# Optimization experiments

Measured on AMD Instinct MI355X. Metric: run time of the kernel, lower is better.

Reference implementation:

```python
import jax, jax.numpy as jnp
import numpy as np

N_ELEC = 8192   # electrons (nodes)
N_NUC = 512     # nuclei
EMB = 256       # embedding_dim
KER = 256       # kernel_dim
DF = 64         # dist_feat_dim
MID = 128       # round(sqrt(DF*KER)), log-interpolated hidden width of w-MLP
E = 131072      # edges per edge type


def _ssp(x):
    # shifted softplus, deepqmc default activation: log(0.5*exp(x) + 0.5)
    return jax.nn.softplus(x) - jnp.log(2.0)


def setup_inputs() -> dict:
    key = jax.random.key(0)
    ks = jax.random.split(key, 24)
    def nrm(k, shape, scale):
        return jax.random.normal(k, shape, dtype=jnp.float32) * scale
    inp = {}
    inp['electrons'] = nrm(ks[0], (N_ELEC, EMB), 1.0)
    inp['nuclei'] = nrm(ks[1], (N_NUC, KER), 1.0)
    for i, lbl in enumerate(['same', 'anti', 'n']):
        inp[f'dist_{lbl}'] = jax.random.uniform(ks[2 + i], (E, DF), dtype=jnp.float32)
        inp[f'w1_{lbl}'] = nrm(ks[5 + i], (DF, MID), DF ** -0.5)
        inp[f'b1_{lbl}'] = jnp.zeros((MID,), jnp.float32)
        inp[f'w2_{lbl}'] = nrm(ks[8 + i], (MID, KER), MID ** -0.5)
        inp[f'g_{lbl}'] = nrm(ks[11 + i], (KER, EMB), KER ** -0.5)
    inp['h_w'] = nrm(ks[14], (EMB, KER), EMB ** -0.5)
    inp['senders_same'] = jax.random.randint(ks[15], (E,), 0, N_ELEC)
    inp['senders_anti'] = jax.random.randint(ks[16], (E,), 0, N_ELEC)
    inp['senders_n'] = jax.random.randint(ks[17], (E,), 0, N_NUC)
    inp['receivers_same'] = jax.random.randint(ks[18], (E,), 0, N_ELEC)
    inp['receivers_anti'] = jax.random.randint(ks[19], (E,), 0, N_ELEC)
    inp['receivers_n'] = jax.random.randint(ks[20], (E,), 0, N_ELEC)
    return inp


def reference(electrons, nuclei, dist_same, dist_anti, dist_n,
              w1_same, b1_same, w2_same, w1_anti, b1_anti, w2_anti,
              w1_n, b1_n, w2_n, g_same, g_anti, g_n, h_w,
              senders_same, senders_anti, senders_n,
              receivers_same, receivers_anti, receivers_n):
    def w_mlp(d, w1, b1, w2):
        # MLP with ('log', 2) hidden layers: linear+bias -> SSP -> last linear (no bias)
        return _ssp(d @ w1 + b1) @ w2

    # per-edge filters from distance features: [E, KER]
    we_same = w_mlp(dist_same, w1_same, b1_same, w2_same)
    we_anti = w_mlp(dist_anti, w1_anti, b1_anti, w2_anti)
    we_n = w_mlp(dist_n, w1_n, b1_n, w2_n)

    # shared h (single bias-free linear) on gathered sender electrons: [E, KER]
    hx_same = electrons[senders_same] @ h_w
    hx_anti = electrons[senders_anti] @ h_w

    weh_same = we_same * hx_same
    weh_anti = we_anti * hx_anti
    weh_n = we_n * nuclei[senders_n]

    # scatter-sum messages to receiver electrons: [N_ELEC, KER]
    z_same = jax.ops.segment_sum(weh_same, receivers_same, num_segments=N_ELEC)
    z_anti = jax.ops.segment_sum(weh_anti, receivers_anti, num_segments=N_ELEC)
    z_n = jax.ops.segment_sum(weh_n, receivers_n, num_segments=N_ELEC)

    # per-label g (single bias-free linear) + residual update, order matches original
    return electrons + (z_n @ g_n + z_same @ g_same + z_anti @ g_anti)
```

## Files before the change

kernel.cpp:

```cpp
#include <hip/hip_runtime.h>
#include <stdint.h>


#define N_ELEC 8192
#define N_NUC  512
#define EMB    256
#define KER    256
#define DF     64
#define MID    128
#define NEDGE  131072
#define RPS    8256
#define CSTR   272

using u16 = unsigned short;
typedef short short8 __attribute__((ext_vector_type(8)));
typedef float f32x4 __attribute__((ext_vector_type(4)));

__device__ __forceinline__ float bf2f(u16 h) {
  return __uint_as_float(((unsigned)h) << 16);
}
__device__ __forceinline__ u16 f2bf(float f) {
  unsigned u = __float_as_uint(f);
  return (u16)((u + 0x7FFFu + ((u >> 16) & 1u)) >> 16);
}
__device__ __forceinline__ unsigned pkbf(float a, float b) {
  return ((unsigned)f2bf(b) << 16) | (unsigned)f2bf(a);
}
__device__ __forceinline__ float ssp_fast(float x) {
  const float e = __expf(-fabsf(x));
  return fmaxf(x, 0.f) + __logf(fmaf(0.5f, e, 0.5f));
}

__device__ __forceinline__ void stage_tile(const char* g0, long stride,
                                           char* lds, int tid) {
  const int l = tid & 63, w = tid >> 6;
#pragma unroll
  for (int c = 0; c < 2; ++c) {
    const int r = c * 64 + w * 16 + (l >> 2);
    const int cb = (l & 3) * 16;
    const char* g = g0 + (long)r * stride + cb;
    char* dst = lds + c * 4096 + w * 1024;
    __builtin_amdgcn_global_load_lds(
        (const __attribute__((address_space(1))) unsigned*)g,
        (__attribute__((address_space(3))) unsigned*)dst, 16, 0, 0);
  }
}

__device__ __forceinline__ void stage_f32(const float* g0, int stride_e,
                                          int kt, char* lds, int tid) {
#pragma unroll
  for (int k = 0; k < 8; ++k) {
    const int idx2 = k * 256 + tid;
    const int row = idx2 >> 4, cp = idx2 & 15;
    const float2 v = *(const float2*)(g0 + (long)row * stride_e + kt + cp * 2);
    *(unsigned*)(lds + row * 64 + cp * 4) = pkbf(v.x, v.y);
  }
}

template <bool A_F32>
__device__ __forceinline__ void gemm_core(const char* A0, long as_bytes,
                                          const float* Af, int as_elems,
                                          const char* B0, long bs, int K,
                                          char* As, char* Bs, f32x4 acc[4][4],
                                          int tid) {
  const int l = tid & 63, lane15 = l & 15, quad = l >> 4, wv = tid >> 6;
  const int mw = (wv >> 1) * 64, nw = (wv & 1) * 64;
  for (int kt = 0; kt < K; kt += 32) {
    if (A_F32)
      stage_f32(Af, as_elems, kt, As, tid);
    else
      stage_tile(A0 + (long)kt * 2, as_bytes, As, tid);
    stage_tile(B0 + (long)kt * 2, bs, Bs, tid);
    __syncthreads();
    short8 af[4], bf[4];
#pragma unroll
    for (int i = 0; i < 4; ++i) {
      af[i] = *(const short8*)(As + (mw + i * 16 + lane15) * 64 + quad * 16);
      bf[i] = *(const short8*)(Bs + (nw + i * 16 + lane15) * 64 + quad * 16);
    }
#pragma unroll
    for (int mi = 0; mi < 4; ++mi)
#pragma unroll
      for (int ni = 0; ni < 4; ++ni)
        acc[mi][ni] = __builtin_amdgcn_mfma_f32_16x16x32_bf16(
            af[mi], bf[ni], acc[mi][ni], 0, 0, 0);
    __syncthreads();
  }
}

__device__ __forceinline__ void zero_acc(f32x4 acc[4][4]) {
#pragma unroll
  for (int i = 0; i < 4; ++i)
#pragma unroll
    for (int j = 0; j < 4; ++j) acc[i][j] = (f32x4){0.f, 0.f, 0.f, 0.f};
}

__global__ __launch_bounds__(256) void k_zeroI(int* cnt) {
  cnt[blockIdx.x * 256 + threadIdx.x] = 0;
}

__global__ __launch_bounds__(256) void k_hist(const int* r0, const int* r1,
                                              const int* r2, int* cnt) {
  const int t = blockIdx.z;
  const int* rcv = t == 0 ? r0 : (t == 1 ? r1 : r2);
  const int e = blockIdx.x * 256 + threadIdx.x;
  atomicAdd(&cnt[t * N_ELEC + rcv[e]], 1);
}

__global__ __launch_bounds__(256) void k_scan(const int* cnt, int* rowptr,
                                              int* cursor) {
  const int t = blockIdx.x, tid = threadIdx.x;
  __shared__ int part[256];
  const int* c = cnt + t * N_ELEC;
  int s = 0;
#pragma unroll
  for (int i = 0; i < 32; ++i) s += c[tid * 32 + i];
  part[tid] = s;
  __syncthreads();
  for (int off = 1; off < 256; off <<= 1) {
    int v = (tid >= off) ? part[tid - off] : 0;
    __syncthreads();
    part[tid] += v;
    __syncthreads();
  }
  int run = (tid == 0) ? 0 : part[tid - 1];
  int* rp = rowptr + t * RPS;
  int* cu = cursor + t * N_ELEC;
  for (int i = 0; i < 32; ++i) {
    rp[tid * 32 + i] = run;
    cu[tid * 32 + i] = run;
    run += c[tid * 32 + i];
  }
  if (tid == 255) rp[N_ELEC] = run;
}

__global__ __launch_bounds__(256) void k_place(const int* r0, const int* r1,
                                               const int* r2, const int* s0,
                                               const int* s1, const int* s2,
                                               int* cursor, int* perm,
                                               int* snd_s, int* rcv_s) {
  const int t = blockIdx.z;
  const int* rcv = t == 0 ? r0 : (t == 1 ? r1 : r2);
  const int* snd = t == 0 ? s0 : (t == 1 ? s1 : s2);
  const int e = blockIdx.x * 256 + threadIdx.x;
  const int rr = rcv[e];
  const int pos = atomicAdd(&cursor[t * N_ELEC + rr], 1);
  perm[t * NEDGE + pos] = e;
  snd_s[t * NEDGE + pos] = snd[e];
  rcv_s[t * NEDGE + pos] = rr;
}

__global__ __launch_bounds__(256) void k_zero(float4* z) {
  z[blockIdx.x * 256 + threadIdx.x] = (float4){0.f, 0.f, 0.f, 0.f};
}

__global__ __launch_bounds__(256) void k_prep(
    const float* h_w, const float* w1s, const float* w1a, const float* w1n,
    const float* w2s, const float* w2a, const float* w2n, const float* gs,
    const float* ga, const float* gn, u16* hwT, u16* w1T, u16* w2T, u16* gT) {
  int i = blockIdx.x * 256 + threadIdx.x;
  if (i < 65536) {
    int n = i >> 8, k = i & 255;
    hwT[i] = f2bf(h_w[k * 256 + n]);
    return;
  }
  int j = i - 65536;
  if (j < 24576) {
    int t = j >> 13, jj = j & 8191, n = jj >> 6, k = jj & 63;
    const float* w1 = t == 0 ? w1s : (t == 1 ? w1a : w1n);
    w1T[j] = f2bf(w1[k * 128 + n]);
    return;
  }
  j -= 24576;
  if (j < 98304) {
    int t = j >> 15, jj = j & 32767, n = jj >> 7, k = jj & 127;
    const float* w2 = t == 0 ? w2s : (t == 1 ? w2a : w2n);
    w2T[j] = f2bf(w2[k * 256 + n]);
    return;
  }
  j -= 98304;
  if (j < 196608) {
    int n = j / 768, q = j % 768, t = q >> 8, k = q & 255;
    const float* g = t == 0 ? gs : (t == 1 ? ga : gn);
    gT[j] = f2bf(g[k * 256 + n]);
  }
}

__global__ __launch_bounds__(256) void k_he(const float* elec, const u16* hwT,
                                            u16* he) {
  __shared__ char As[8192], Bs[8192];
  f32x4 acc[4][4];
  zero_acc(acc);
  const int m0 = blockIdx.x * 128, n0 = blockIdx.y * 128;
  gemm_core<true>(nullptr, 0, elec + (long)m0 * 256, 256,
                  (const char*)hwT + (long)n0 * 512, 512, 256, As, Bs, acc,
                  threadIdx.x);
  const int l = threadIdx.x & 63, lane15 = l & 15, quad = l >> 4,
            wv = threadIdx.x >> 6;
  const int mw = (wv >> 1) * 64, nw = (wv & 1) * 64;
#pragma unroll
  for (int mi = 0; mi < 4; ++mi)
#pragma unroll
    for (int r = 0; r < 4; ++r) {
      const int row = m0 + mw + mi * 16 + quad * 4 + r;
#pragma unroll
      for (int ni = 0; ni < 4; ++ni) {
        const int col = n0 + nw + ni * 16 + lane15;
        he[row * 256 + col] = f2bf(acc[mi][ni][r]);
      }
    }
}

__global__ __launch_bounds__(256) void k_mlp1(
    const float* d0, const float* d1, const float* d2, const float* b0,
    const float* b1p, const float* b2, const u16* w1T, const int* perm,
    u16* midact) {
  __shared__ char As[2][8192];
  const int t = blockIdx.z;
  const float* dist = t == 0 ? d0 : (t == 1 ? d1 : d2);
  const float* bias = t == 0 ? b0 : (t == 1 ? b1p : b2);
  const u16* w1t = w1T + t * 8192;
  const int m0 = blockIdx.x * 128;
  const int tid = threadIdx.x;

  int rows[4];
  const int* pm = perm + t * NEDGE + m0;
#pragma unroll
  for (int s = 0; s < 4; ++s) rows[s] = pm[(s * 256 + tid) >> 3];
#pragma unroll
  for (int j = 0; j < 2; ++j)
#pragma unroll
    for (int s = 0; s < 4; ++s) {
      const int idx = s * 256 + tid, row = idx >> 3, ch = idx & 7;
      const float4 v =
          *(const float4*)(dist + (long)rows[s] * 64 + j * 32 + ch * 4);
      uint2 p;
      p.x = pkbf(v.x, v.y);
      p.y = pkbf(v.z, v.w);
      *(uint2*)(As[j] + row * 64 + ch * 8) = p;
    }
  __syncthreads();

  const int l = tid & 63, lane15 = l & 15, quad = l >> 4, wv = tid >> 6;
  const int mw = (wv >> 1) * 64, nw = (wv & 1) * 64;
  f32x4 acc[4][4];
  zero_acc(acc);
#pragma unroll
  for (int j = 0; j < 2; ++j) {
    short8 af[4], bf[4];
#pragma unroll
    for (int i = 0; i < 4; ++i) {
      af[i] = *(const short8*)(As[j] + (mw + i * 16 + lane15) * 64 + quad * 16);
      bf[i] = *(const short8*)(w1t + (nw + i * 16 + lane15) * 64 + j * 32 +
                               quad * 8);
    }
#pragma unroll
    for (int mi = 0; mi < 4; ++mi)
#pragma unroll
      for (int ni = 0; ni < 4; ++ni)
        acc[mi][ni] = __builtin_amdgcn_mfma_f32_16x16x32_bf16(
            af[mi], bf[ni], acc[mi][ni], 0, 0, 0);
  }

  u16* mout = midact + (size_t)t * ((size_t)NEDGE * MID);
#pragma unroll
  for (int mi = 0; mi < 4; ++mi)
#pragma unroll
    for (int r = 0; r < 4; ++r) {
      const int row = m0 + mw + mi * 16 + quad * 4 + r;
#pragma unroll
      for (int ni = 0; ni < 4; ++ni) {
        const int col = nw + ni * 16 + lane15;
        const float x = acc[mi][ni][r] + bias[col];
        mout[(size_t)row * MID + col] = f2bf(ssp_fast(x));
      }
    }
}

__global__ __launch_bounds__(256) void k_wz(const u16* midact, const u16* w2T,
                                            const u16* he, const float* nucf,
                                            const int* snd_s, const int* rcv_s,
                                            float* z) {
  __shared__ char smem[128 * CSTR + 1024];
  int* snd_l = (int*)(smem + 128 * CSTR);
  int* rcv_l = snd_l + 128;

  const int t = blockIdx.z;
  const int m0 = blockIdx.x * 128, n0 = blockIdx.y * 128;
  const int tid = threadIdx.x;
  const bool is_nuc = (t == 2);
  const u16* midact_t = midact + (size_t)t * ((size_t)NEDGE * MID);
  const u16* w2T_t = w2T + t * 32768;

  if (tid < 128)
    snd_l[tid] = snd_s[t * NEDGE + m0 + tid];
  else
    rcv_l[tid - 128] = rcv_s[t * NEDGE + m0 + tid - 128];

  f32x4 acc[4][4];
  zero_acc(acc);
  gemm_core<false>((const char*)midact_t + (long)m0 * 256, 256, nullptr, 0,
                   (const char*)w2T_t + (long)n0 * 256, 256, 128, smem,
                   smem + 8192, acc, tid);

  u16* HeC = (u16*)smem;
  if (!is_nuc) {
#pragma unroll
    for (int c = 0; c < 8; ++c) {
      const int chunk = c * 256 + tid;
      const int row = chunk >> 4, off = chunk & 15;
      const uint4 v = *(const uint4*)((const char*)he +
                                      (size_t)snd_l[row] * 512 + n0 * 2 +
                                      off * 16);
      *(uint4*)((char*)HeC + row * CSTR + off * 16) = v;
    }
  } else {
#pragma unroll
    for (int c = 0; c < 8; ++c) {
      const int chunk = c * 256 + tid;
      const int row = chunk >> 4, off = chunk & 15;
      const char* src =
          (const char*)nucf + (size_t)snd_l[row] * 1024 + n0 * 4 + off * 32;
      const float4 a = *(const float4*)src;
      const float4 b = *(const float4*)(src + 16);
      uint4 p;
      p.x = pkbf(a.x, a.y);
      p.y = pkbf(a.z, a.w);
      p.z = pkbf(b.x, b.y);
      p.w = pkbf(b.z, b.w);
      *(uint4*)((char*)HeC + row * CSTR + off * 16) = p;
    }
  }
  __syncthreads();

  const int l = tid & 63, lane15 = l & 15, quad = l >> 4, wv = tid >> 6;
  const int mw = (wv >> 1) * 64, nw = (wv & 1) * 64;
#pragma unroll
  for (int mi = 0; mi < 4; ++mi)
#pragma unroll
    for (int r = 0; r < 4; ++r) {
      const int row = mw + mi * 16 + quad * 4 + r;
#pragma unroll
      for (int ni = 0; ni < 4; ++ni) {
        const int col = nw + ni * 16 + lane15;
        u16* p = (u16*)((char*)HeC + row * CSTR) + col;
        *p = f2bf(acc[mi][ni][r] * bf2f(*p));
      }
    }
  __syncthreads();

  {
    const int cp = l;
    const int rbeg = wv * 32, rend = rbeg + 32;
    float a0 = 0.f, a1 = 0.f;
    int cur = rcv_l[rbeg];
    for (int row = rbeg; row < rend; ++row) {
      const unsigned p = *(const unsigned*)((char*)HeC + row * CSTR + cp * 4);
      a0 += __uint_as_float(p << 16);
      a1 += __uint_as_float(p & 0xffff0000u);
      const int nxt = (row + 1 < rend) ? rcv_l[row + 1] : -1;
      if (nxt != cur) {
        float* zp = z + (size_t)cur * 768 + t * 256 + n0 + cp * 2;
        unsafeAtomicAdd(zp, a0);
        unsafeAtomicAdd(zp + 1, a1);
        a0 = a1 = 0.f;
        cur = nxt;
      }
    }
  }
}

__global__ __launch_bounds__(256) void k_final(const float* z, const u16* gT,
                                               const float* elec, float* out) {
  __shared__ char As[8192], Bs[8192];
  f32x4 acc[4][4];
  zero_acc(acc);
  const int m0 = blockIdx.x * 128, n0 = blockIdx.y * 128;
  gemm_core<true>(nullptr, 0, z + (long)m0 * 768, 768,
                  (const char*)gT + (long)n0 * 1536, 1536, 768, As, Bs, acc,
                  threadIdx.x);
  const int l = threadIdx.x & 63, lane15 = l & 15, quad = l >> 4,
            wv = threadIdx.x >> 6;
  const int mw = (wv >> 1) * 64, nw = (wv & 1) * 64;
#pragma unroll
  for (int mi = 0; mi < 4; ++mi)
#pragma unroll
    for (int r = 0; r < 4; ++r) {
      const int row = m0 + mw + mi * 16 + quad * 4 + r;
#pragma unroll
      for (int ni = 0; ni < 4; ++ni) {
        const int col = n0 + nw + ni * 16 + lane15;
        out[row * 256 + col] = acc[mi][ni][r] + elec[row * 256 + col];
      }
    }
}

extern "C" void kernel_launch(void* const* d_in, const int* in_sizes, int n_in,
                              void* d_out, int out_size, void* d_ws,
                              size_t ws_size, hipStream_t stream) {
  int I_dist[3], I_w1[3], I_b1[3], I_w2[3], I_g[3], I_hw;
  if (in_sizes[3] == 64 * 128) {
    for (int t = 0; t < 3; ++t) {
      I_dist[t] = 2 + t * 5 + 0;
      I_w1[t] = 2 + t * 5 + 1;
      I_b1[t] = 2 + t * 5 + 2;
      I_w2[t] = 2 + t * 5 + 3;
      I_g[t] = 2 + t * 5 + 4;
    }
    I_hw = 17;
  } else {
    I_dist[0] = 2; I_dist[1] = 3; I_dist[2] = 4;
    I_w1[0] = 5;  I_b1[0] = 6;  I_w2[0] = 7;
    I_w1[1] = 8;  I_b1[1] = 9;  I_w2[1] = 10;
    I_w1[2] = 11; I_b1[2] = 12; I_w2[2] = 13;
    I_g[0] = 14; I_g[1] = 15; I_g[2] = 16;
    I_hw = 17;
  }
  const int I_snd[3] = {18, 19, 20};
  const int I_rcv[3] = {21, 22, 23};

  char* ws = (char*)d_ws;
  u16* he = (u16*)(ws + 0);
  u16* hwT = (u16*)(ws + 4194304);
  u16* w1T = (u16*)(ws + 4325376);
  u16* w2T = (u16*)(ws + 4374528);
  u16* gT = (u16*)(ws + 4571136);
  u16* midact = (u16*)(ws + 4964352);
  float* z = (float*)(ws + 105627648);
  int* cnt = (int*)(ws + 130793472);
  int* rowptr = (int*)(ws + 130891776);
  int* cursor = (int*)(ws + 130990848);
  int* perm = (int*)(ws + 131089152);
  int* snd_s = (int*)(ws + 132662016);
  int* rcv_s = (int*)(ws + 134234880);

  const float* elec = (const float*)d_in[0];
  const float* nuc = (const float*)d_in[1];
  const int* s0 = (const int*)d_in[I_snd[0]];
  const int* s1 = (const int*)d_in[I_snd[1]];
  const int* s2 = (const int*)d_in[I_snd[2]];
  const int* r0 = (const int*)d_in[I_rcv[0]];
  const int* r1 = (const int*)d_in[I_rcv[1]];
  const int* r2 = (const int*)d_in[I_rcv[2]];

  k_zeroI<<<3 * N_ELEC / 256, 256, 0, stream>>>(cnt);
  k_hist<<<dim3(NEDGE / 256, 1, 3), 256, 0, stream>>>(r0, r1, r2, cnt);
  k_scan<<<3, 256, 0, stream>>>(cnt, rowptr, cursor);
  k_place<<<dim3(NEDGE / 256, 1, 3), 256, 0, stream>>>(r0, r1, r2, s0, s1, s2,
                                                       cursor, perm, snd_s,
                                                       rcv_s);

  k_zero<<<(N_ELEC * 768 / 4) / 256, 256, 0, stream>>>((float4*)z);

  k_prep<<<1504, 256, 0, stream>>>(
      (const float*)d_in[I_hw], (const float*)d_in[I_w1[0]],
      (const float*)d_in[I_w1[1]], (const float*)d_in[I_w1[2]],
      (const float*)d_in[I_w2[0]], (const float*)d_in[I_w2[1]],
      (const float*)d_in[I_w2[2]], (const float*)d_in[I_g[0]],
      (const float*)d_in[I_g[1]], (const float*)d_in[I_g[2]], hwT, w1T, w2T,
      gT);

  k_he<<<dim3(N_ELEC / 128, 2), 256, 0, stream>>>(elec, hwT, he);

  k_mlp1<<<dim3(NEDGE / 128, 1, 3), 256, 0, stream>>>(
      (const float*)d_in[I_dist[0]], (const float*)d_in[I_dist[1]],
      (const float*)d_in[I_dist[2]], (const float*)d_in[I_b1[0]],
      (const float*)d_in[I_b1[1]], (const float*)d_in[I_b1[2]], w1T, perm,
      midact);

  k_wz<<<dim3(NEDGE / 128, 2, 3), 256, 0, stream>>>(midact, w2T, he, nuc,
                                                    snd_s, rcv_s, z);

  k_final<<<dim3(N_ELEC / 128, 2), 256, 0, stream>>>(z, gT, elec,
                                                     (float*)d_out);
}
```

Measured before the change: 464.8 us.

## Fuse edge MLP first layer into filter-scatter kernel, keep hidden activations in LDS

Merges k_mlp1 and k_wz into one k_edge kernel. The SSP hidden activations now stay in shared memory instead of round-tripping through a ~100MB bf16 global buffer. Each block loops over both 128-column halves of the output, so the first layer is computed once per edge tile rather than the midact tile being reloaded twice. It also combines the z and count zeroing kernels into one launch. The cost is fewer blocks (the y dimension of the grid is gone), more LDS per block (~70KB), which lowers occupancy, and serialized work within each block.

```diff
diff --git a/kernel.cpp b/kernel.cpp
--- a/kernel.cpp
+++ b/kernel.cpp
@@ -95,8 +95,12 @@
     for (int j = 0; j < 4; ++j) acc[i][j] = (f32x4){0.f, 0.f, 0.f, 0.f};
 }
 
-__global__ __launch_bounds__(256) void k_zeroI(int* cnt) {
-  cnt[blockIdx.x * 256 + threadIdx.x] = 0;
+__global__ __launch_bounds__(256) void k_zero2(float4* z, int* cnt) {
+  const int b = blockIdx.x;
+  if (b < 6144)
+    z[b * 256 + threadIdx.x] = (float4){0.f, 0.f, 0.f, 0.f};
+  else
+    cnt[(b - 6144) * 256 + threadIdx.x] = 0;
 }
 
 __global__ __launch_bounds__(256) void k_hist(const int* r0, const int* r1,
@@ -150,10 +154,6 @@
   rcv_s[t * NEDGE + pos] = rr;
 }
 
-__global__ __launch_bounds__(256) void k_zero(float4* z) {
-  z[blockIdx.x * 256 + threadIdx.x] = (float4){0.f, 0.f, 0.f, 0.f};
-}
-
 __global__ __launch_bounds__(256) void k_prep(
     const float* h_w, const float* w1s, const float* w1a, const float* w1n,
     const float* w2s, const float* w2a, const float* w2n, const float* gs,
@@ -211,17 +211,28 @@
     }
 }
 
-__global__ __launch_bounds__(256) void k_mlp1(
+__global__ __launch_bounds__(256) void k_edge(
     const float* d0, const float* d1, const float* d2, const float* b0,
-    const float* b1p, const float* b2, const u16* w1T, const int* perm,
-    u16* midact) {
-  __shared__ char As[2][8192];
+    const float* b1p, const float* b2, const u16* w1T, const u16* w2T,
+    const u16* he, const float* nucf, const int* perm, const int* snd_s,
+    const int* rcv_s, float* z) {
+  __shared__ char mid[128 * CSTR];
+  __shared__ char buf[128 * CSTR];
+  __shared__ int snd_l[128], rcv_l[128];
+
   const int t = blockIdx.z;
+  const int m0 = blockIdx.x * 128;
+  const int tid = threadIdx.x;
   const float* dist = t == 0 ? d0 : (t == 1 ? d1 : d2);
   const float* bias = t == 0 ? b0 : (t == 1 ? b1p : b2);
   const u16* w1t = w1T + t * 8192;
-  const int m0 = blockIdx.x * 128;
-  const int tid = threadIdx.x;
+  const u16* w2t = w2T + t * 32768;
+  const bool is_nuc = (t == 2);
+
+  if (tid < 128)
+    snd_l[tid] = snd_s[t * NEDGE + m0 + tid];
+  else
+    rcv_l[tid - 128] = rcv_s[t * NEDGE + m0 + tid - 128];
 
   int rows[4];
   const int* pm = perm + t * NEDGE + m0;
@@ -237,12 +248,13 @@
       uint2 p;
       p.x = pkbf(v.x, v.y);
       p.y = pkbf(v.z, v.w);
-      *(uint2*)(As[j] + row * 64 + ch * 8) = p;
+      *(uint2*)(buf + j * 8192 + row * 64 + ch * 8) = p;
     }
   __syncthreads();
 
   const int l = tid & 63, lane15 = l & 15, quad = l >> 4, wv = tid >> 6;
   const int mw = (wv >> 1) * 64, nw = (wv & 1) * 64;
+
   f32x4 acc[4][4];
   zero_acc(acc);
 #pragma unroll
@@ -250,7 +262,8 @@
     short8 af[4], bf[4];
 #pragma unroll
     for (int i = 0; i < 4; ++i) {
-      af[i] = *(const short8*)(As[j] + (mw + i * 16 + lane15) * 64 + quad * 16);
+      af[i] = *(const short8*)(buf + j * 8192 + (mw + i * 16 + lane15) * 64 +
+                               quad * 16);
       bf[i] = *(const short8*)(w1t + (nw + i * 16 + lane15) * 64 + j * 32 +
                                quad * 8);
     }
@@ -261,112 +274,106 @@
         acc[mi][ni] = __builtin_amdgcn_mfma_f32_16x16x32_bf16(
             af[mi], bf[ni], acc[mi][ni], 0, 0, 0);
   }
-
-  u16* mout = midact + (size_t)t * ((size_t)NEDGE * MID);
+  __syncthreads();
+
 #pragma unroll
   for (int mi = 0; mi < 4; ++mi)
 #pragma unroll
     for (int r = 0; r < 4; ++r) {
-      const int row = m0 + mw + mi * 16 + quad * 4 + r;
+      const int row = mw + mi * 16 + quad * 4 + r;
 #pragma unroll
       for (int ni = 0; ni < 4; ++ni) {
         const int col = nw + ni * 16 + lane15;
         const float x = acc[mi][ni][r] + bias[col];
-        mout[(size_t)row * MID + col] = f2bf(ssp_fast(x));
-      }
-    }
-}
-
-__global__ __launch_bounds__(256) void k_wz(const u16* midact, const u16* w2T,
-                                            const u16* he, const float* nucf,
-                                            const int* snd_s, const int* rcv_s,
-                                            float* z) {
-  __shared__ char smem[128 * CSTR + 1024];
-  int* snd_l = (int*)(smem + 128 * CSTR);
-  int* rcv_l = snd_l + 128;
-
-  const int t = blockIdx.z;
-  const int m0 = blockIdx.x * 128, n0 = blockIdx.y * 128;
-  const int tid = threadIdx.x;
-  const bool is_nuc = (t == 2);
-  const u16* midact_t = midact + (size_t)t * ((size_t)NEDGE * MID);
-  const u16* w2T_t = w2T + t * 32768;
-
-  if (tid < 128)
-    snd_l[tid] = snd_s[t * NEDGE + m0 + tid];
-  else
-    rcv_l[tid - 128] = rcv_s[t * NEDGE + m0 + tid - 128];
-
-  f32x4 acc[4][4];
-  zero_acc(acc);
-  gemm_core<false>((const char*)midact_t + (long)m0 * 256, 256, nullptr, 0,
-                   (const char*)w2T_t + (long)n0 * 256, 256, 128, smem,
-                   smem + 8192, acc, tid);
-
-  u16* HeC = (u16*)smem;
-  if (!is_nuc) {
-#pragma unroll
-    for (int c = 0; c < 8; ++c) {
-      const int chunk = c * 256 + tid;
-      const int row = chunk >> 4, off = chunk & 15;
-      const uint4 v = *(const uint4*)((const char*)he +
-                                      (size_t)snd_l[row] * 512 + n0 * 2 +
-                                      off * 16);
-      *(uint4*)((char*)HeC + row * CSTR + off * 16) = v;
-    }
-  } else {
-#pragma unroll
-    for (int c = 0; c < 8; ++c) {
-      const int chunk = c * 256 + tid;
-      const int row = chunk >> 4, off = chunk & 15;
-      const char* src =
-          (const char*)nucf + (size_t)snd_l[row] * 1024 + n0 * 4 + off * 32;
-      const float4 a = *(const float4*)src;
-      const float4 b = *(const float4*)(src + 16);
-      uint4 p;
-      p.x = pkbf(a.x, a.y);
-      p.y = pkbf(a.z, a.w);
-      p.z = pkbf(b.x, b.y);
-      p.w = pkbf(b.z, b.w);
-      *(uint4*)((char*)HeC + row * CSTR + off * 16) = p;
-    }
-  }
+        *(u16*)(mid + row * CSTR + col * 2) = f2bf(ssp_fast(x));
+      }
+    }
   __syncthreads();
 
-  const int l = tid & 63, lane15 = l & 15, quad = l >> 4, wv = tid >> 6;
-  const int mw = (wv >> 1) * 64, nw = (wv & 1) * 64;
-#pragma unroll
-  for (int mi = 0; mi < 4; ++mi)
-#pragma unroll
-    for (int r = 0; r < 4; ++r) {
-      const int row = mw + mi * 16 + quad * 4 + r;
-#pragma unroll
-      for (int ni = 0; ni < 4; ++ni) {
-        const int col = nw + ni * 16 + lane15;
-        u16* p = (u16*)((char*)HeC + row * CSTR) + col;
-        *p = f2bf(acc[mi][ni][r] * bf2f(*p));
-      }
-    }
-  __syncthreads();
-
-  {
-    const int cp = l;
-    const int rbeg = wv * 32, rend = rbeg + 32;
-    float a0 = 0.f, a1 = 0.f;
-    int cur = rcv_l[rbeg];
-    for (int row = rbeg; row < rend; ++row) {
-      const unsigned p = *(const unsigned*)((char*)HeC + row * CSTR + cp * 4);
-      a0 += __uint_as_float(p << 16);
-      a1 += __uint_as_float(p & 0xffff0000u);
-      const int nxt = (row + 1 < rend) ? rcv_l[row + 1] : -1;
-      if (nxt != cur) {
-        float* zp = z + (size_t)cur * 768 + t * 256 + n0 + cp * 2;
-        unsafeAtomicAdd(zp, a0);
-        unsafeAtomicAdd(zp + 1, a1);
-        a0 = a1 = 0.f;
-        cur = nxt;
-      }
-    }
+  u16* HeC = (u16*)buf;
+  for (int n0 = 0; n0 < 256; n0 += 128) {
+    zero_acc(acc);
+#pragma unroll
+    for (int kt = 0; kt < 128; kt += 32) {
+      short8 af[4], bf[4];
+#pragma unroll
+      for (int i = 0; i < 4; ++i) {
+        af[i] = *(const short8*)(mid + (mw + i * 16 + lane15) * CSTR + kt * 2 +
+                                 quad * 16);
+        bf[i] = *(const short8*)(w2t + (n0 + nw + i * 16 + lane15) * 128 + kt +
+                                 quad * 8);
+      }
+#pragma unroll
+      for (int mi = 0; mi < 4; ++mi)
+#pragma unroll
+        for (int ni = 0; ni < 4; ++ni)
+          acc[mi][ni] = __builtin_amdgcn_mfma_f32_16x16x32_bf16(
+              af[mi], bf[ni], acc[mi][ni], 0, 0, 0);
+    }
+
+    if (!is_nuc) {
+#pragma unroll
+      for (int c = 0; c < 8; ++c) {
+        const int chunk = c * 256 + tid;
+        const int row = chunk >> 4, off = chunk & 15;
+        const uint4 v = *(const uint4*)((const char*)he +
+                                        (size_t)snd_l[row] * 512 + n0 * 2 +
+                                        off * 16);
+        *(uint4*)((char*)HeC + row * CSTR + off * 16) = v;
+      }
+    } else {
+#pragma unroll
+      for (int c = 0; c < 8; ++c) {
+        const int chunk = c * 256 + tid;
+        const int row = chunk >> 4, off = chunk & 15;
+        const char* src =
+            (const char*)nucf + (size_t)snd_l[row] * 1024 + n0 * 4 + off * 32;
+        const float4 a = *(const float4*)src;
+        const float4 b = *(const float4*)(src + 16);
+        uint4 p;
+        p.x = pkbf(a.x, a.y);
+        p.y = pkbf(a.z, a.w);
+        p.z = pkbf(b.x, b.y);
+        p.w = pkbf(b.z, b.w);
+        *(uint4*)((char*)HeC + row * CSTR + off * 16) = p;
+      }
+    }
+    __syncthreads();
+
+#pragma unroll
+    for (int mi = 0; mi < 4; ++mi)
+#pragma unroll
+      for (int r = 0; r < 4; ++r) {
+        const int row = mw + mi * 16 + quad * 4 + r;
+#pragma unroll
+        for (int ni = 0; ni < 4; ++ni) {
+          const int col = nw + ni * 16 + lane15;
+          u16* p = (u16*)((char*)HeC + row * CSTR) + col;
+          *p = f2bf(acc[mi][ni][r] * bf2f(*p));
+        }
+      }
+    __syncthreads();
+
+    {
+      const int cp = l;
+      const int rbeg = wv * 32, rend = rbeg + 32;
+      float a0 = 0.f, a1 = 0.f;
+      int cur = rcv_l[rbeg];
+      for (int row = rbeg; row < rend; ++row) {
+        const unsigned p = *(const unsigned*)((char*)HeC + row * CSTR + cp * 4);
+        a0 += __uint_as_float(p << 16);
+        a1 += __uint_as_float(p & 0xffff0000u);
+        const int nxt = (row + 1 < rend) ? rcv_l[row + 1] : -1;
+        if (nxt != cur) {
+          float* zp = z + (size_t)cur * 768 + t * 256 + n0 + cp * 2;
+          unsafeAtomicAdd(zp, a0);
+          unsafeAtomicAdd(zp + 1, a1);
+          a0 = a1 = 0.f;
+          cur = nxt;
+        }
+      }
+    }
+    __syncthreads();
   }
 }
 
@@ -425,14 +432,13 @@
   u16* w1T = (u16*)(ws + 4325376);
   u16* w2T = (u16*)(ws + 4374528);
   u16* gT = (u16*)(ws + 4571136);
-  u16* midact = (u16*)(ws + 4964352);
-  float* z = (float*)(ws + 105627648);
-  int* cnt = (int*)(ws + 130793472);
-  int* rowptr = (int*)(ws + 130891776);
-  int* cursor = (int*)(ws + 130990848);
-  int* perm = (int*)(ws + 131089152);
-  int* snd_s = (int*)(ws + 132662016);
-  int* rcv_s = (int*)(ws + 134234880);
+  float* z = (float*)(ws + 4964352);
+  int* cnt = (int*)(ws + 30130176);
+  int* rowptr = (int*)(ws + 30228480);
+  int* cursor = (int*)(ws + 30327552);
+  int* perm = (int*)(ws + 30425856);
+  int* snd_s = (int*)(ws + 31998720);
+  int* rcv_s = (int*)(ws + 33571584);
 
   const float* elec = (const float*)d_in[0];
   const float* nuc = (const float*)d_in[1];
@@ -443,14 +449,13 @@
   const int* r1 = (const int*)d_in[I_rcv[1]];
   const int* r2 = (const int*)d_in[I_rcv[2]];
 
-  k_zeroI<<<3 * N_ELEC / 256, 256, 0, stream>>>(cnt);
+  k_zero2<<<6240, 256, 0, stream>>>((float4*)z, cnt);
+
   k_hist<<<dim3(NEDGE / 256, 1, 3), 256, 0, stream>>>(r0, r1, r2, cnt);
   k_scan<<<3, 256, 0, stream>>>(cnt, rowptr, cursor);
   k_place<<<dim3(NEDGE / 256, 1, 3), 256, 0, stream>>>(r0, r1, r2, s0, s1, s2,
                                                        cursor, perm, snd_s,
                                                        rcv_s);
-
-  k_zero<<<(N_ELEC * 768 / 4) / 256, 256, 0, stream>>>((float4*)z);
 
   k_prep<<<1504, 256, 0, stream>>>(
       (const float*)d_in[I_hw], (const float*)d_in[I_w1[0]],
@@ -462,14 +467,11 @@
 
   k_he<<<dim3(N_ELEC / 128, 2), 256, 0, stream>>>(elec, hwT, he);
 
-  k_mlp1<<<dim3(NEDGE / 128, 1, 3), 256, 0, stream>>>(
+  k_edge<<<dim3(NEDGE / 128, 1, 3), 256, 0, stream>>>(
       (const float*)d_in[I_dist[0]], (const float*)d_in[I_dist[1]],
       (const float*)d_in[I_dist[2]], (const float*)d_in[I_b1[0]],
-      (const float*)d_in[I_b1[1]], (const float*)d_in[I_b1[2]], w1T, perm,
-      midact);
-
-  k_wz<<<dim3(NEDGE / 128, 2, 3), 256, 0, stream>>>(midact, w2T, he, nuc,
-                                                    snd_s, rcv_s, z);
+      (const float*)d_in[I_b1[1]], (const float*)d_in[I_b1[2]], w1T, w2T, he,
+      nuc, perm, snd_s, rcv_s, z);
 
   k_final<<<dim3(N_ELEC / 128, 2), 256, 0, stream>>>(z, gT, elec,
                                                      (float*)d_out);
```

Measured after the change: 436.1 us. 1.07x faster.
